# Kernel optimization log

Measured on AMD Instinct MI355X. Metric: run time of the kernel, lower is better.

## Reference

```python
import jax, jax.numpy as jnp
import numpy as np

K = 20
EPS = 1e-5

def lrelu(y):
    return jnp.where(y >= 0, y, 0.2 * y)

def bn(y, g, b):
    # inference BatchNorm, running_mean=0, running_var=1; channel axis = 1 (or -1 for 2D)
    shape = (1, -1) + (1,) * (y.ndim - 2)
    return y * (g / jnp.sqrt(1.0 + EPS)).reshape(shape) + b.reshape(shape)

def get_graph_feature(x, k):
    # x: (B, C, N) -> edge features (B, N, k, 2C) = concat(nbr - ctr, ctr)
    xt = jnp.swapaxes(x, 1, 2)                     # (B, N, C)
    xx = jnp.sum(xt * xt, axis=-1)                 # (B, N)
    inner = jnp.einsum('bnc,bmc->bnm', xt, xt)     # (B, N, N)
    dist = 2.0 * inner - xx[:, :, None] - xx[:, None, :]  # = -||xi-xj||^2
    idx = jax.lax.top_k(dist, k)[1]                # (B, N, k) nearest (incl. self)
    nbr = jax.vmap(lambda f, i: f[i])(xt, idx)     # (B, N, k, C)
    ctr = jnp.broadcast_to(xt[:, :, None, :], nbr.shape)
    return jnp.concatenate([nbr - ctr, ctr], axis=-1)

def edge_block(x, W, g, b, k):
    # 1x1 conv on edge features + BN + LeakyReLU + max over neighbors
    e = get_graph_feature(x, k)                    # (B, N, k, 2C)
    y = jnp.einsum('bnkc,oc->bonk', e, W)          # (B, O, N, k)
    y = lrelu(bn(y, g, b))
    return jnp.max(y, axis=-1)                     # (B, O, N)

def setup_inputs() -> dict:
    key = jax.random.key(0)
    ks = jax.random.split(key, 32)
    B, C, N = 16, 3, 2048
    s = 0.05
    d = {}
    d['x'] = jax.random.normal(ks[0], (B, C, N), dtype=jnp.float32)
    d['W1'] = jax.random.normal(ks[1], (64, 6), dtype=jnp.float32) * s
    d['W2'] = jax.random.normal(ks[2], (64, 128), dtype=jnp.float32) * s
    d['W3'] = jax.random.normal(ks[3], (128, 128), dtype=jnp.float32) * s
    d['W4'] = jax.random.normal(ks[4], (256, 256), dtype=jnp.float32) * s
    d['W5'] = jax.random.normal(ks[5], (1024, 512), dtype=jnp.float32) * s
    for i, c in zip(range(1, 8), [64, 64, 128, 256, 1024, 512, 256]):
        d[f'g{i}'] = jnp.ones((c,), jnp.float32) + jax.random.normal(ks[5 + i], (c,)) * 0.01
        d[f'b{i}'] = jax.random.normal(ks[12 + i], (c,)) * 0.01
    d['L1w'] = jax.random.normal(ks[20], (512, 2048), dtype=jnp.float32) * s
    d['L2w'] = jax.random.normal(ks[21], (256, 512), dtype=jnp.float32) * s
    d['L2b'] = jnp.zeros((256,), jnp.float32)
    d['L3w'] = jax.random.normal(ks[22], (40, 256), dtype=jnp.float32) * s
    d['L3b'] = jnp.zeros((40,), jnp.float32)
    return d

def reference(x, W1, W2, W3, W4, W5,
              g1, b1, g2, b2, g3, b3, g4, b4, g5, b5, g6, b6, g7, b7,
              L1w, L2w, L2b, L3w, L3b):
    x1 = edge_block(x, W1, g1, b1, K)       # (B, 64, N)
    x2 = edge_block(x1, W2, g2, b2, K)      # (B, 64, N)
    x3 = edge_block(x2, W3, g3, b3, K)      # (B, 128, N)
    x4 = edge_block(x3, W4, g4, b4, K)      # (B, 256, N)
    xc = jnp.concatenate([x1, x2, x3, x4], axis=1)      # (B, 512, N)
    y = lrelu(bn(jnp.einsum('bcn,oc->bon', xc, W5), g5, b5))  # (B, 1024, N)
    p = jnp.concatenate([jnp.max(y, axis=-1), jnp.mean(y, axis=-1)], axis=1)  # (B, 2048)
    h = lrelu(bn(p @ L1w.T, g6, b6))
    h = lrelu(bn(h @ L2w.T + L2b, g7, b7))
    return h @ L3w.T + L3b                  # (B, 40)
```

## Files before the change

### kernel.cpp

```cpp
#include <hip/hip_runtime.h>
#include <cstdint>
#include <cstddef>

#define RSQ 0.9999950000374997f
#define LDL 132
#define PITCH 40

typedef __attribute__((ext_vector_type(8))) short bf16x8;
typedef __attribute__((ext_vector_type(4))) float f32x4;

__device__ __forceinline__ float lrelu_f(float x){ return x >= 0.0f ? x : 0.2f * x; }

__device__ __forceinline__ float bf2f(unsigned short u){
  union{unsigned int i; float f;} v; v.i = ((unsigned int)u) << 16; return v.f;
}
__device__ __forceinline__ void splitbf(float x, unsigned short& h, unsigned short& l){
  union{float f; unsigned int i;} a; a.f = x;
  unsigned int r = a.i + 0x7fffu + ((a.i >> 16) & 1u);
  h = (unsigned short)(r >> 16);
  union{unsigned int i; float f;} hf; hf.i = ((unsigned int)h) << 16;
  union{float f; unsigned int i;} b; b.f = x - hf.f;
  unsigned int r2 = b.i + 0x7fffu + ((b.i >> 16) & 1u);
  l = (unsigned short)(r2 >> 16);
}

__device__ __forceinline__ unsigned long long packkey(float v, int m){
  union{float f; unsigned int i;} a; a.f = v;
  unsigned int s = a.i;
  unsigned int u = s ^ (((unsigned int)((int)s >> 31)) | 0x80000000u);
  return ((unsigned long long)u << 32) | (unsigned int)(2047 - m);
}

__device__ __forceinline__ unsigned long long bitonic64_asc(unsigned long long v, int lane){
  #pragma unroll
  for (int k = 2; k <= 64; k <<= 1){
    #pragma unroll
    for (int j = k >> 1; j > 0; j >>= 1){
      unsigned long long o = __shfl_xor(v, j);
      bool up = ((lane & k) == 0);
      bool upper = (lane & j) != 0;
      unsigned long long mx = v > o ? v : o;
      unsigned long long mn = v > o ? o : v;
      v = (upper == up) ? mx : mn;
    }
  }
  return v;
}


__global__ __launch_bounds__(256) void k_transpose(const float* __restrict__ x, float* __restrict__ F0){
  int t = blockIdx.x * 256 + threadIdx.x;
  if (t >= 16*3*2048) return;
  int n = t & 2047;
  int bc = t >> 11;
  int c = bc % 3, b = bc / 3;
  F0[(size_t)(b*2048 + n)*3 + c] = x[t];
}

__global__ __launch_bounds__(256) void k_split_plain(const float* __restrict__ W, int n,
    unsigned short* __restrict__ H, unsigned short* __restrict__ L){
  int t = blockIdx.x * 256 + threadIdx.x;
  if (t >= n) return;
  unsigned short h, l; splitbf(W[t], h, l);
  H[t] = h; L[t] = l;
}

__global__ __launch_bounds__(256) void k_make_wuz(const float* __restrict__ W, int O, int cshift,
    unsigned short* __restrict__ WH, unsigned short* __restrict__ WL){
  int C = 1 << cshift;
  int n = 2*O*C;
  int t = blockIdx.x * 256 + threadIdx.x;
  if (t >= n) return;
  int g = t >> cshift, c = t & (C - 1);
  int C2 = 2*C;
  float w;
  if (g < O) w = W[(size_t)g*C2 + c];
  else       w = W[(size_t)(g-O)*C2 + C + c] - W[(size_t)(g-O)*C2 + c];
  unsigned short h, l; splitbf(w, h, l);
  WH[t] = h; WL[t] = l;
}

__global__ __launch_bounds__(256) void k_norms_bf(const unsigned short* __restrict__ H,
    const unsigned short* __restrict__ L, int c0, int C, float* __restrict__ xx){
  int row = blockIdx.x * 256 + threadIdx.x;
  const unsigned short* h = H + (size_t)row*512 + c0;
  const unsigned short* l = L + (size_t)row*512 + c0;
  float a = 0.f;
  for (int c = 0; c < C; c += 8){
    bf16x8 vh = *(const bf16x8*)(h + c);
    bf16x8 vl = *(const bf16x8*)(l + c);
    #pragma unroll
    for (int j = 0; j < 8; ++j){
      float f = bf2f((unsigned short)vh[j]) + bf2f((unsigned short)vl[j]);
      a += f*f;
    }
  }
  xx[row] = a;
}


__device__ __forceinline__ void stage_pair(unsigned short* dH, unsigned short* dL,
    const unsigned short* sH, const unsigned short* sL, int rowBase, int ld, int kOff, int tid){
  #pragma unroll
  for (int i = 0; i < 2; ++i){
    int q = tid + 256*i; int r = q >> 2; int kq = (q & 3) * 8;
    size_t go = (size_t)(rowBase + r)*ld + kOff + kq;
    *(bf16x8*)&dH[r*PITCH + kq] = *(const bf16x8*)(sH + go);
    *(bf16x8*)&dL[r*PITCH + kq] = *(const bf16x8*)(sL + go);
  }
}

__device__ __forceinline__ void mfma_step(const unsigned short* sAh, const unsigned short* sAl,
    const unsigned short* sBh, const unsigned short* sBl, int wm, int wn, int lane, f32x4 acc[4][4]){
  bf16x8 ah[4], al[4], bh[4], bl[4];
  int ko = (lane >> 4) * 8, li = lane & 15;
  #pragma unroll
  for (int i = 0; i < 4; ++i){
    ah[i] = *(const bf16x8*)&sAh[(wm + i*16 + li)*PITCH + ko];
    al[i] = *(const bf16x8*)&sAl[(wm + i*16 + li)*PITCH + ko];
    bh[i] = *(const bf16x8*)&sBh[(wn + i*16 + li)*PITCH + ko];
    bl[i] = *(const bf16x8*)&sBl[(wn + i*16 + li)*PITCH + ko];
  }
  #pragma unroll
  for (int mi = 0; mi < 4; ++mi){
    #pragma unroll
    for (int ni = 0; ni < 4; ++ni){
      acc[mi][ni] = __builtin_amdgcn_mfma_f32_16x16x32_bf16(ah[mi], bh[ni], acc[mi][ni], 0,0,0);
      acc[mi][ni] = __builtin_amdgcn_mfma_f32_16x16x32_bf16(ah[mi], bl[ni], acc[mi][ni], 0,0,0);
      acc[mi][ni] = __builtin_amdgcn_mfma_f32_16x16x32_bf16(al[mi], bh[ni], acc[mi][ni], 0,0,0);
    }
  }
}

__global__ __launch_bounds__(256) void k_dist_mfma(const unsigned short* __restrict__ H,
    const unsigned short* __restrict__ L, int C, const float* __restrict__ xx,
    float* __restrict__ D, int b0){
  __shared__ unsigned short sAh[128*PITCH], sAl[128*PITCH], sBh[128*PITCH], sBl[128*PITCH];
  int b = b0 + blockIdx.z;
  int nb = blockIdx.y * 128, mb = blockIdx.x * 128;
  int rowA0 = b*2048 + nb, rowB0 = b*2048 + mb;
  int tid = threadIdx.x, lane = tid & 63, w = tid >> 6;
  int wm = (w >> 1) * 64, wn = (w & 1) * 64;
  f32x4 acc[4][4];
  #pragma unroll
  for (int i = 0; i < 4; ++i)
    #pragma unroll
    for (int j = 0; j < 4; ++j){ f32x4 z = {0.f,0.f,0.f,0.f}; acc[i][j] = z; }
  for (int kk = 0; kk < C; kk += 32){
    __syncthreads();
    stage_pair(sAh, sAl, H, L, rowA0, 512, kk, tid);
    stage_pair(sBh, sBl, H, L, rowB0, 512, kk, tid);
    __syncthreads();
    mfma_step(sAh, sAl, sBh, sBl, wm, wn, lane, acc);
  }
  int li = lane & 15, lq = lane >> 4;
  float xm[4];
  #pragma unroll
  for (int ni = 0; ni < 4; ++ni) xm[ni] = xx[rowB0 + wn + ni*16 + li];
  #pragma unroll
  for (int mi = 0; mi < 4; ++mi){
    #pragma unroll
    for (int v = 0; v < 4; ++v){
      int row = wm + mi*16 + lq*4 + v;
      float xn = xx[rowA0 + row];
      size_t base = ((size_t)(blockIdx.z*2048 + nb + row))*2048 + mb;
      #pragma unroll
      for (int ni = 0; ni < 4; ++ni){
        D[base + wn + ni*16 + li] = 2.f*acc[mi][ni][v] - xn - xm[ni];
      }
    }
  }
}

__global__ __launch_bounds__(256) void k_uz_mfma(const unsigned short* __restrict__ H,
    const unsigned short* __restrict__ L, int C,
    const unsigned short* __restrict__ WH, const unsigned short* __restrict__ WL,
    int N2, float* __restrict__ UZ){
  __shared__ unsigned short sAh[128*PITCH], sAl[128*PITCH], sBh[128*PITCH], sBl[128*PITCH];
  int rows0 = blockIdx.x * 128;
  int ob = blockIdx.y * 128;
  int tid = threadIdx.x, lane = tid & 63, w = tid >> 6;
  int wm = (w >> 1) * 64, wn = (w & 1) * 64;
  f32x4 acc[4][4];
  #pragma unroll
  for (int i = 0; i < 4; ++i)
    #pragma unroll
    for (int j = 0; j < 4; ++j){ f32x4 z = {0.f,0.f,0.f,0.f}; acc[i][j] = z; }
  for (int kk = 0; kk < C; kk += 32){
    __syncthreads();
    stage_pair(sAh, sAl, H, L, rows0, 512, kk, tid);
    stage_pair(sBh, sBl, WH, WL, ob, C, kk, tid);
    __syncthreads();
    mfma_step(sAh, sAl, sBh, sBl, wm, wn, lane, acc);
  }
  int li = lane & 15, lq = lane >> 4;
  #pragma unroll
  for (int mi = 0; mi < 4; ++mi){
    #pragma unroll
    for (int v = 0; v < 4; ++v){
      int row = rows0 + wm + mi*16 + lq*4 + v;
      size_t base = (size_t)row * N2 + ob;
      #pragma unroll
      for (int ni = 0; ni < 4; ++ni) UZ[base + wn + ni*16 + li] = acc[mi][ni][v];
    }
  }
}

__global__ __launch_bounds__(256) void k_conv5_mfma(const unsigned short* __restrict__ XH,
    const unsigned short* __restrict__ XL, const unsigned short* __restrict__ WH,
    const unsigned short* __restrict__ WL, const float* __restrict__ g5, const float* __restrict__ b5,
    float* __restrict__ pmax, float* __restrict__ psum){
  __shared__ unsigned short sAh[128*PITCH], sAl[128*PITCH], sBh[128*PITCH], sBl[128*PITCH];
  __shared__ float redm[2][128];
  __shared__ float reds[2][128];
  int bx = blockIdx.x;
  int b = bx >> 4, nt = bx & 15;
  int ob = blockIdx.y * 128;
  int rowA0 = b*2048 + nt*128;
  int tid = threadIdx.x, lane = tid & 63, w = tid >> 6;
  int wm = (w >> 1) * 64, wn = (w & 1) * 64, wy = w >> 1, wx = w & 1;
  f32x4 acc[4][4];
  #pragma unroll
  for (int i = 0; i < 4; ++i)
    #pragma unroll
    for (int j = 0; j < 4; ++j){ f32x4 z = {0.f,0.f,0.f,0.f}; acc[i][j] = z; }
  for (int kk = 0; kk < 512; kk += 32){
    __syncthreads();
    stage_pair(sAh, sAl, XH, XL, rowA0, 512, kk, tid);
    stage_pair(sBh, sBl, WH, WL, ob, 512, kk, tid);
    __syncthreads();
    mfma_step(sAh, sAl, sBh, sBl, wm, wn, lane, acc);
  }
  int li = lane & 15;
  #pragma unroll
  for (int ni = 0; ni < 4; ++ni){
    int c = ob + wn + ni*16 + li;
    float s = g5[c] * RSQ, bb = b5[c];
    float m = -INFINITY, sm = 0.f;
    #pragma unroll
    for (int mi = 0; mi < 4; ++mi){
      #pragma unroll
      for (int v = 0; v < 4; ++v){
        float y = lrelu_f(s*acc[mi][ni][v] + bb);
        m = fmaxf(m, y);
        sm += y;
      }
    }
    m = fmaxf(m, __shfl_xor(m, 16)); m = fmaxf(m, __shfl_xor(m, 32));
    sm += __shfl_xor(sm, 16); sm += __shfl_xor(sm, 32);
    if (lane < 16){
      redm[wy][wx*64 + ni*16 + li] = m;
      reds[wy][wx*64 + ni*16 + li] = sm;
    }
  }
  __syncthreads();
  if (tid < 128){
    float m = fmaxf(redm[0][tid], redm[1][tid]);
    float s = reds[0][tid] + reds[1][tid];
    size_t pi = (size_t)(b*16 + nt)*1024 + ob + tid;
    pmax[pi] = m;
    psum[pi] = s;
  }
}


__global__ __launch_bounds__(256) void k_dist3(const float* __restrict__ F0, float* __restrict__ D, int b0){
  __shared__ float sa[3][128];
  __shared__ float sb[3][128];
  int b = b0 + blockIdx.z;
  int nb = blockIdx.y * 128, mb = blockIdx.x * 128;
  int tid = threadIdx.x, tx = tid & 15, ty = tid >> 4;
  if (tid < 128){
    int r = tid;
    const float* p = F0 + (size_t)(b*2048 + nb + r)*3;
    sa[0][r] = p[0]; sa[1][r] = p[1]; sa[2][r] = p[2];
  } else {
    int r = tid - 128;
    const float* p = F0 + (size_t)(b*2048 + mb + r)*3;
    sb[0][r] = p[0]; sb[1][r] = p[1]; sb[2][r] = p[2];
  }
  __syncthreads();
  float ax[8], ay[8], az[8], bx[8], by[8], bz[8];
  #pragma unroll
  for (int i=0;i<8;i++){
    int ri = (i<4) ? 4*ty+i : 64 + 4*ty + (i-4);
    ax[i] = sa[0][ri]; ay[i] = sa[1][ri]; az[i] = sa[2][ri];
    int cj = (i<4) ? 4*tx+i : 64 + 4*tx + (i-4);
    bx[i] = sb[0][cj]; by[i] = sb[1][cj]; bz[i] = sb[2][cj];
  }
  #pragma unroll
  for (int i=0;i<8;i++){
    int ri = (i<4) ? 4*ty+i : 64 + 4*ty + (i-4);
    size_t base = ((size_t)(blockIdx.z*2048 + nb + ri))*2048 + mb;
    float v[8];
    #pragma unroll
    for (int j=0;j<8;j++){
      float dx = ax[i]-bx[j], dy = ay[i]-by[j], dz = az[i]-bz[j];
      v[j] = -(dx*dx + dy*dy + dz*dz);
    }
    *(float4*)&D[base + 4*tx]      = make_float4(v[0],v[1],v[2],v[3]);
    *(float4*)&D[base + 64 + 4*tx] = make_float4(v[4],v[5],v[6],v[7]);
  }
}

#define GEMM_STEP(KK) { \
      float a[8], wv_[8]; \
      *(float4*)&a[0] = *(const float4*)&As[(KK)*LDL + 4*ty]; \
      *(float4*)&a[4] = *(const float4*)&As[(KK)*LDL + 64 + 4*ty]; \
      *(float4*)&wv_[0] = *(const float4*)&Bs[(KK)*LDL + 4*tx]; \
      *(float4*)&wv_[4] = *(const float4*)&Bs[(KK)*LDL + 64 + 4*tx]; \
      _Pragma("unroll") \
      for (int i_ = 0; i_ < 8; ++i_){ \
        _Pragma("unroll") \
        for (int j_ = 0; j_ < 8; ++j_) acc[i_][j_] += a[i_]*wv_[j_]; \
      } }

__global__ __launch_bounds__(256) void k_uz(const float* __restrict__ F, int ldF, int C,
    const float* __restrict__ W, int O, float* __restrict__ UZ){
  __shared__ float As[32*LDL];
  __shared__ float Bs[32*LDL];
  int N2 = 2*O, C2 = 2*C;
  int rows0 = blockIdx.x * 128;
  int ob = blockIdx.y * 128;
  int tid = threadIdx.x, tx = tid & 15, ty = tid >> 4;
  float acc[8][8] = {};
  for (int cc = 0; cc < C; cc += 32){
    int kc = C - cc; if (kc > 32) kc = 32;
    __syncthreads();
    for (int t = tid; t < 128*32; t += 256){
      int r = t >> 5, k = t & 31;
      if (k < kc){
        As[k*LDL + r] = F[(size_t)(rows0 + r)*ldF + cc + k];
        int g = ob + r; float wv;
        if (g < O) wv = W[(size_t)g*C2 + cc + k];
        else       wv = W[(size_t)(g-O)*C2 + C + cc + k] - W[(size_t)(g-O)*C2 + cc + k];
        Bs[k*LDL + r] = wv;
      }
    }
    __syncthreads();
    for (int k = 0; k < kc; ++k) GEMM_STEP(k)
  }
  #pragma unroll
  for (int i=0;i<8;i++){
    int ri = (i<4) ? 4*ty+i : 64 + 4*ty + (i-4);
    size_t base = (size_t)(rows0 + ri)*N2 + ob;
    *(float4*)&UZ[base + 4*tx]      = make_float4(acc[i][0],acc[i][1],acc[i][2],acc[i][3]);
    *(float4*)&UZ[base + 64 + 4*tx] = make_float4(acc[i][4],acc[i][5],acc[i][6],acc[i][7]);
  }
}


__global__ __launch_bounds__(256) void k_knn_select(const float* __restrict__ D, int* __restrict__ idxo, int b0){
  __shared__ unsigned long long cand[4][64];
  int g = blockIdx.y; int b = b0 + g;
  int w = threadIdx.x >> 6, lane = threadIdx.x & 63;
  int r = blockIdx.x*4 + w;
  const float* Drow = D + ((size_t)(g*2048 + r))*2048;
  float vals[32];
  unsigned long long kmax = 0ull;
  #pragma unroll
  for (int j=0;j<32;j++){
    float v = Drow[j*64 + lane];
    vals[j] = v;
    unsigned long long ke = packkey(v, j*64 + lane);
    if (ke > kmax) kmax = ke;
  }
  unsigned long long srt = bitonic64_asc(kmax, lane);
  unsigned long long t = __shfl(srt, 44);
  unsigned long long ltmask = (1ull << lane) - 1ull;
  int base = 0;
  #pragma unroll
  for (int j=0;j<32;j++){
    unsigned long long ke = packkey(vals[j], j*64 + lane);
    bool pred = ke >= t;
    unsigned long long mask = __ballot(pred);
    int pos = base + __popcll(mask & ltmask);
    if (pred && pos < 64) cand[w][pos] = ke;
    base += __popcll(mask);
  }
  int* op = idxo + (size_t)(b*2048 + r)*20;
  if (base <= 64){
    unsigned long long ck = (lane < base) ? cand[w][lane] : 0ull;
    ck = bitonic64_asc(ck, lane);
    if (lane >= 44) op[63 - lane] = 2047 - (int)(ck & 0xFFFFFFFFull);
  } else {
    unsigned long long k1 = 0ull, k2 = 0ull;
    #pragma unroll
    for (int j=0;j<32;j++){
      unsigned long long ke = packkey(vals[j], j*64 + lane);
      if (ke > k1){ k2 = k1; k1 = ke; }
      else if (ke > k2){ k2 = ke; }
    }
    unsigned int removed = 0u;
    for (int it = 0; it < 20; ++it){
      unsigned long long km = k1;
      #pragma unroll
      for (int off = 1; off < 64; off <<= 1){
        unsigned long long o2 = __shfl_xor(km, off);
        if (o2 > km) km = o2;
      }
      int bi = 2047 - (int)(km & 0xFFFFFFFFull);
      if (lane == 0) op[it] = bi;
      if (km == k1){
        removed |= 1u << (bi >> 6);
        if (k2 != 0ull){ k1 = k2; k2 = 0ull; }
        else {
          unsigned long long b1 = 0ull, b2 = 0ull;
          #pragma unroll
          for (int j=0;j<32;j++){
            if (!((removed >> j) & 1u)){
              unsigned long long ke = packkey(vals[j], j*64 + lane);
              if (ke > b1){ b2 = b1; b1 = ke; }
              else if (ke > b2){ b2 = ke; }
            }
          }
          k1 = b1; k2 = b2;
        }
      }
    }
  }
}

__global__ __launch_bounds__(256) void k_aggregate(const float* __restrict__ UZ,
    const int* __restrict__ idx, const float* __restrict__ gam, const float* __restrict__ bet,
    int oshift, unsigned short* __restrict__ outH, unsigned short* __restrict__ outL){
  int O = 1 << oshift;
  int ogshift = oshift - 2;
  int tid = threadIdx.x;
  int NBB = gridDim.x >> 4;
  int g = blockIdx.x;
  int q = g >> 3, xq = g & 7;
  int hi = (q >= NBB) ? 1 : 0;
  int within = q - NBB*hi;
  int batch = xq + 8*hi;
  int pblock = batch * NBB + within;
  int point = pblock * (256 >> ogshift) + (tid >> ogshift);
  int o = (tid & ((O >> 2) - 1)) << 2;
  int N2 = 2*O;
  int b = point >> 11;
  const int* ip = idx + (size_t)point * 20;
  float4 mv = make_float4(-INFINITY,-INFINITY,-INFINITY,-INFINITY);
  #pragma unroll
  for (int j = 0; j < 20; ++j){
    int m = ip[j];
    float4 v = *(const float4*)(UZ + (size_t)((b << 11) + m)*N2 + o);
    mv.x = fmaxf(mv.x, v.x); mv.y = fmaxf(mv.y, v.y);
    mv.z = fmaxf(mv.z, v.z); mv.w = fmaxf(mv.w, v.w);
  }
  float4 z = *(const float4*)(UZ + (size_t)point*N2 + O + o);
  float s0 = gam[o+0]*RSQ, s1 = gam[o+1]*RSQ, s2 = gam[o+2]*RSQ, s3 = gam[o+3]*RSQ;
  float y0 = lrelu_f(s0*(mv.x + z.x) + bet[o+0]);
  float y1 = lrelu_f(s1*(mv.y + z.y) + bet[o+1]);
  float y2 = lrelu_f(s2*(mv.z + z.z) + bet[o+2]);
  float y3 = lrelu_f(s3*(mv.w + z.w) + bet[o+3]);
  ushort4 hh, ll;
  splitbf(y0, hh.x, ll.x); splitbf(y1, hh.y, ll.y);
  splitbf(y2, hh.z, ll.z); splitbf(y3, hh.w, ll.w);
  *(ushort4*)&outH[(size_t)point*512 + o] = hh;
  *(ushort4*)&outL[(size_t)point*512 + o] = ll;
}

__global__ __launch_bounds__(256) void k_pool(const float* __restrict__ pmax, const float* __restrict__ psum,
    float* __restrict__ p){
  int t = blockIdx.x * 256 + threadIdx.x;
  int b = t >> 10, o = t & 1023;
  float m = -INFINITY, s = 0.f;
  for (int nt = 0; nt < 16; ++nt){
    size_t pi = (size_t)(b*16 + nt)*1024 + o;
    m = fmaxf(m, pmax[pi]);
    s += psum[pi];
  }
  p[(size_t)b*2048 + o] = m;
  p[(size_t)b*2048 + 1024 + o] = s * (1.f/2048.f);
}

__global__ __launch_bounds__(256) void k_fc1(const float* __restrict__ p, const float* __restrict__ L1w,
    const float* __restrict__ g6, const float* __restrict__ b6, float* __restrict__ h1){
  int o = blockIdx.x;
  int tid = threadIdx.x, lane = tid & 63, w = tid >> 6;
  int k0 = w*512 + lane*8;
  const float4* wp = (const float4*)(L1w + (size_t)o*2048 + k0);
  float4 w0 = wp[0], w1 = wp[1];
  __shared__ float part[4][16];
  for (int b = 0; b < 16; ++b){
    const float4* pp = (const float4*)(p + (size_t)b*2048 + k0);
    float4 p0 = pp[0], p1 = pp[1];
    float a = p0.x*w0.x + p0.y*w0.y + p0.z*w0.z + p0.w*w0.w
            + p1.x*w1.x + p1.y*w1.y + p1.z*w1.z + p1.w*w1.w;
    #pragma unroll
    for (int off = 32; off >= 1; off >>= 1) a += __shfl_down(a, off);
    if (lane == 0) part[w][b] = a;
  }
  __syncthreads();
  if (tid < 16){
    float a = part[0][tid] + part[1][tid] + part[2][tid] + part[3][tid];
    h1[(size_t)tid*512 + o] = lrelu_f(g6[o]*RSQ*a + b6[o]);
  }
}

__global__ __launch_bounds__(256) void k_fc2(const float* __restrict__ h1, const float* __restrict__ L2w,
    const float* __restrict__ L2b, const float* __restrict__ g7, const float* __restrict__ b7,
    float* __restrict__ h2){
  int o = blockIdx.x;
  int tid = threadIdx.x, lane = tid & 63, w = tid >> 6;
  int k0 = w*128 + lane*2;
  float2 wv = *(const float2*)(L2w + (size_t)o*512 + k0);
  __shared__ float part[4][16];
  for (int b = 0; b < 16; ++b){
    float2 hv = *(const float2*)(h1 + (size_t)b*512 + k0);
    float a = hv.x*wv.x + hv.y*wv.y;
    #pragma unroll
    for (int off = 32; off >= 1; off >>= 1) a += __shfl_down(a, off);
    if (lane == 0) part[w][b] = a;
  }
  __syncthreads();
  if (tid < 16){
    float a = part[0][tid] + part[1][tid] + part[2][tid] + part[3][tid] + L2b[o];
    h2[(size_t)tid*256 + o] = lrelu_f(g7[o]*RSQ*a + b7[o]);
  }
}

__global__ __launch_bounds__(256) void k_fc3(const float* __restrict__ h2, const float* __restrict__ L3w,
    const float* __restrict__ L3b, float* __restrict__ out){
  int o = blockIdx.x;
  int tid = threadIdx.x, lane = tid & 63, w = tid >> 6;
  int k0 = w*64 + lane;
  float wv = L3w[(size_t)o*256 + k0];
  __shared__ float part[4][16];
  for (int b = 0; b < 16; ++b){
    float a = h2[(size_t)b*256 + k0] * wv;
    #pragma unroll
    for (int off = 32; off >= 1; off >>= 1) a += __shfl_down(a, off);
    if (lane == 0) part[w][b] = a;
  }
  __syncthreads();
  if (tid < 16){
    float a = part[0][tid] + part[1][tid] + part[2][tid] + part[3][tid] + L3b[o];
    out[(size_t)tid*40 + o] = a;
  }
}

extern "C" void kernel_launch(void* const* d_in, const int* in_sizes, int n_in,
                              void* d_out, int out_size, void* d_ws, size_t ws_size,
                              hipStream_t stream) {
  (void)in_sizes; (void)n_in; (void)out_size;
  const float* x   = (const float*)d_in[0];
  const float* W1  = (const float*)d_in[1];
  const float* W2  = (const float*)d_in[2];
  const float* W3  = (const float*)d_in[3];
  const float* W4  = (const float*)d_in[4];
  const float* W5  = (const float*)d_in[5];
  const float* g1  = (const float*)d_in[6];   const float* b1  = (const float*)d_in[7];
  const float* g2  = (const float*)d_in[8];   const float* b2  = (const float*)d_in[9];
  const float* g3  = (const float*)d_in[10];  const float* b3  = (const float*)d_in[11];
  const float* g4  = (const float*)d_in[12];  const float* b4  = (const float*)d_in[13];
  const float* g5  = (const float*)d_in[14];  const float* b5  = (const float*)d_in[15];
  const float* g6  = (const float*)d_in[16];  const float* b6  = (const float*)d_in[17];
  const float* g7  = (const float*)d_in[18];  const float* b7  = (const float*)d_in[19];
  const float* L1w = (const float*)d_in[20];
  const float* L2w = (const float*)d_in[21];  const float* L2b = (const float*)d_in[22];
  const float* L3w = (const float*)d_in[23];  const float* L3b = (const float*)d_in[24];
  float* out = (float*)d_out;

  char* ws = (char*)d_ws;
  size_t off = 0;
  auto alloc = [&](size_t nbytes) -> void* {
    void* pp = (void*)(ws + off);
    off += (nbytes + 255) & ~(size_t)255;
    return pp;
  };
  float*          F0   = (float*)alloc(98304ull * 4);
  unsigned short* XCH  = (unsigned short*)alloc(16777216ull * 2);
  unsigned short* XCL  = (unsigned short*)alloc(16777216ull * 2);
  float*          UZ   = (float*)alloc(16777216ull * 4);
  float*          XX   = (float*)alloc(32768ull * 4);
  int*            IDX  = (int*)alloc(655360ull * 4);
  float*          PM   = (float*)alloc(262144ull * 4);
  float*          PS   = (float*)alloc(262144ull * 4);
  float*          P    = (float*)alloc(32768ull * 4);
  float*          H1   = (float*)alloc(8192ull * 4);
  float*          H2   = (float*)alloc(4096ull * 4);
  unsigned short* W5H  = (unsigned short*)alloc(524288ull * 2);
  unsigned short* W5L  = (unsigned short*)alloc(524288ull * 2);
  unsigned short* WUZH = (unsigned short*)alloc(65536ull * 2);
  unsigned short* WUZL = (unsigned short*)alloc(65536ull * 2);
  const size_t dbytes = 2048ull * 2048ull * 4ull;
  size_t rem = (ws_size > off) ? (ws_size - off) : 0;
  int G = (int)(rem / dbytes);
  if (G > 8) G = 8;
  if (G < 1) G = 1;
  float* Dbuf = (float*)(ws + off);

  k_transpose<<<dim3(384), dim3(256), 0, stream>>>(x, F0);
  k_split_plain<<<dim3(2048), dim3(256), 0, stream>>>(W5, 524288, W5H, W5L);

  struct Blk { int c0; int C; int cshift; const float* W; const float* g; const float* bb; int O; int oshift; int c0out; };
  Blk cfg[4] = {
    { 0,   3,   0, W1, g1, b1, 64,  6, 0   },
    { 0,   64,  6, W2, g2, b2, 64,  6, 64  },
    { 64,  64,  6, W3, g3, b3, 128, 7, 128 },
    { 128, 128, 7, W4, g4, b4, 256, 8, 256 },
  };

  for (int blk = 0; blk < 4; ++blk){
    const Blk& c = cfg[blk];
    if (blk > 0){
      k_make_wuz<<<dim3((2*c.O*c.C + 255)/256), dim3(256), 0, stream>>>(c.W, c.O, c.cshift, WUZH, WUZL);
      k_norms_bf<<<dim3(128), dim3(256), 0, stream>>>(XCH, XCL, c.c0, c.C, XX);
    }
    for (int b0 = 0; b0 < 16; b0 += G){
      int Gc = 16 - b0; if (Gc > G) Gc = G;
      if (blk == 0)
        k_dist3<<<dim3(16, 16, Gc), dim3(256), 0, stream>>>(F0, Dbuf, b0);
      else
        k_dist_mfma<<<dim3(16, 16, Gc), dim3(256), 0, stream>>>(XCH + c.c0, XCL + c.c0, c.C, XX, Dbuf, b0);
      k_knn_select<<<dim3(512, Gc), dim3(256), 0, stream>>>(Dbuf, IDX, b0);
    }
    if (blk == 0)
      k_uz<<<dim3(256, 1), dim3(256), 0, stream>>>(F0, 3, 3, c.W, c.O, UZ);
    else
      k_uz_mfma<<<dim3(256, (2*c.O)/128), dim3(256), 0, stream>>>(XCH + c.c0, XCL + c.c0, c.C, WUZH, WUZL, 2*c.O, UZ);
    k_aggregate<<<dim3(32768 >> (8 - (c.oshift - 2))), dim3(256), 0, stream>>>(UZ, IDX, c.g, c.bb, c.oshift,
                                                                         XCH + c.c0out, XCL + c.c0out);
  }

  k_conv5_mfma<<<dim3(256, 8), dim3(256), 0, stream>>>(XCH, XCL, W5H, W5L, g5, b5, PM, PS);
  k_pool<<<dim3(64), dim3(256), 0, stream>>>(PM, PS, P);
  k_fc1<<<dim3(512), dim3(256), 0, stream>>>(P, L1w, g6, b6, H1);
  k_fc2<<<dim3(256), dim3(256), 0, stream>>>(H1, L2w, L2b, g7, b7, H2);
  k_fc3<<<dim3(40),  dim3(256), 0, stream>>>(H2, L3w, L3b, out);
}
```

Measured before the change: 941.8 us.

## Exploit distance-matrix symmetry and vectorize kNN row loads

The MFMA distance kernel now computes only the upper-triangular 128x128 tiles (136 per batch instead of 256). Each off-diagonal tile is also written transposed, staged through padded shared memory, so the full matrix is still produced. This roughly halves the matrix-multiply work and the operand loads. The kNN selection kernel now reads each row with float4 loads and remaps its element and removed-mask indexing to the new per-lane layout. The cost is extra LDS traffic, barriers and a second full store pass per off-diagonal tile.

New measurement: 964.2 us. 2.4% more time.

```diff
diff --git a/kernel.cpp b/kernel.cpp
--- a/kernel.cpp
+++ b/kernel.cpp
@@ -132,12 +132,21 @@
   }
 }
 
-__global__ __launch_bounds__(256) void k_dist_mfma(const unsigned short* __restrict__ H,
+__global__ __launch_bounds__(256) void k_dist_sym(const unsigned short* __restrict__ H,
     const unsigned short* __restrict__ L, int C, const float* __restrict__ xx,
     float* __restrict__ D, int b0){
-  __shared__ unsigned short sAh[128*PITCH], sAl[128*PITCH], sBh[128*PITCH], sBl[128*PITCH];
-  int b = b0 + blockIdx.z;
-  int nb = blockIdx.y * 128, mb = blockIdx.x * 128;
+  __shared__ unsigned short sstage[4*128*PITCH];
+  unsigned short* sAh = sstage;
+  unsigned short* sAl = sstage + 128*PITCH;
+  unsigned short* sBh = sstage + 2*128*PITCH;
+  unsigned short* sBl = sstage + 3*128*PITCH;
+  float* tbuf = (float*)sstage;
+  int rem = blockIdx.x;
+  int ti = 0;
+  while (rem >= 16 - ti){ rem -= 16 - ti; ++ti; }
+  int tj = ti + rem;
+  int b = b0 + blockIdx.y;
+  int nb = ti*128, mb = tj*128;
   int rowA0 = b*2048 + nb, rowB0 = b*2048 + mb;
   int tid = threadIdx.x, lane = tid & 63, w = tid >> 6;
   int wm = (w >> 1) * 64, wn = (w & 1) * 64;
@@ -163,10 +172,32 @@
     for (int v = 0; v < 4; ++v){
       int row = wm + mi*16 + lq*4 + v;
       float xn = xx[rowA0 + row];
-      size_t base = ((size_t)(blockIdx.z*2048 + nb + row))*2048 + mb;
+      size_t base = ((size_t)(blockIdx.y*2048 + nb + row))*2048 + mb;
       #pragma unroll
       for (int ni = 0; ni < 4; ++ni){
-        D[base + wn + ni*16 + li] = 2.f*acc[mi][ni][v] - xn - xm[ni];
+        float fv = 2.f*acc[mi][ni][v] - xn - xm[ni];
+        acc[mi][ni][v] = fv;
+        D[base + wn + ni*16 + li] = fv;
+      }
+    }
+  }
+  if (ti != tj){
+    float* tb = tbuf + (w & 1) * (64*65);
+    #pragma unroll
+    for (int pass = 0; pass < 2; ++pass){
+      __syncthreads();
+      if ((w >> 1) == pass){
+        #pragma unroll
+        for (int mi = 0; mi < 4; ++mi)
+          #pragma unroll
+          for (int ni = 0; ni < 4; ++ni)
+            #pragma unroll
+            for (int v = 0; v < 4; ++v)
+              tb[(mi*16 + lq*4 + v)*65 + ni*16 + li] = acc[mi][ni][v];
+        for (int r2 = 0; r2 < 64; ++r2){
+          size_t rb = ((size_t)(blockIdx.y*2048 + mb + wn + r2))*2048 + nb + wm;
+          D[rb + lane] = tb[lane*65 + r2];
+        }
       }
     }
   }
@@ -359,19 +390,24 @@
   float vals[32];
   unsigned long long kmax = 0ull;
   #pragma unroll
-  for (int j=0;j<32;j++){
-    float v = Drow[j*64 + lane];
-    vals[j] = v;
-    unsigned long long ke = packkey(v, j*64 + lane);
-    if (ke > kmax) kmax = ke;
+  for (int j=0;j<8;j++){
+    float4 v4 = *(const float4*)(Drow + j*256 + lane*4);
+    int m0 = j*256 + lane*4;
+    vals[j*4+0]=v4.x; vals[j*4+1]=v4.y; vals[j*4+2]=v4.z; vals[j*4+3]=v4.w;
+    unsigned long long e;
+    e = packkey(v4.x, m0+0); if (e > kmax) kmax = e;
+    e = packkey(v4.y, m0+1); if (e > kmax) kmax = e;
+    e = packkey(v4.z, m0+2); if (e > kmax) kmax = e;
+    e = packkey(v4.w, m0+3); if (e > kmax) kmax = e;
   }
   unsigned long long srt = bitonic64_asc(kmax, lane);
   unsigned long long t = __shfl(srt, 44);
   unsigned long long ltmask = (1ull << lane) - 1ull;
   int base = 0;
   #pragma unroll
-  for (int j=0;j<32;j++){
-    unsigned long long ke = packkey(vals[j], j*64 + lane);
+  for (int s=0;s<32;s++){
+    int m = (s >> 2)*256 + lane*4 + (s & 3);
+    unsigned long long ke = packkey(vals[s], m);
     bool pred = ke >= t;
     unsigned long long mask = __ballot(pred);
     int pos = base + __popcll(mask & ltmask);
@@ -386,8 +422,9 @@
   } else {
     unsigned long long k1 = 0ull, k2 = 0ull;
     #pragma unroll
-    for (int j=0;j<32;j++){
-      unsigned long long ke = packkey(vals[j], j*64 + lane);
+    for (int s=0;s<32;s++){
+      int m = (s >> 2)*256 + lane*4 + (s & 3);
+      unsigned long long ke = packkey(vals[s], m);
       if (ke > k1){ k2 = k1; k1 = ke; }
       else if (ke > k2){ k2 = ke; }
     }
@@ -402,14 +439,15 @@
       int bi = 2047 - (int)(km & 0xFFFFFFFFull);
       if (lane == 0) op[it] = bi;
       if (km == k1){
-        removed |= 1u << (bi >> 6);
+        removed |= 1u << (((bi >> 8) << 2) | (bi & 3));
         if (k2 != 0ull){ k1 = k2; k2 = 0ull; }
         else {
           unsigned long long b1 = 0ull, b2 = 0ull;
           #pragma unroll
-          for (int j=0;j<32;j++){
-            if (!((removed >> j) & 1u)){
-              unsigned long long ke = packkey(vals[j], j*64 + lane);
+          for (int s=0;s<32;s++){
+            if (!((removed >> s) & 1u)){
+              int m = (s >> 2)*256 + lane*4 + (s & 3);
+              unsigned long long ke = packkey(vals[s], m);
               if (ke > b1){ b2 = b1; b1 = ke; }
               else if (ke > b2){ b2 = ke; }
             }
@@ -613,7 +651,7 @@
       if (blk == 0)
         k_dist3<<<dim3(16, 16, Gc), dim3(256), 0, stream>>>(F0, Dbuf, b0);
       else
-        k_dist_mfma<<<dim3(16, 16, Gc), dim3(256), 0, stream>>>(XCH + c.c0, XCL + c.c0, c.C, XX, Dbuf, b0);
+        k_dist_sym<<<dim3(136, Gc), dim3(256), 0, stream>>>(XCH + c.c0, XCL + c.c0, c.C, XX, Dbuf, b0);
       k_knn_select<<<dim3(512, Gc), dim3(256), 0, stream>>>(Dbuf, IDX, b0);
     }
     if (blk == 0)
```
